# Performance work log

Measured on AMD Instinct MI355X. Metric: run time of the kernel, lower is better.

## Reference

```python
import jax, jax.numpy as jnp
import numpy as np
from jax import lax

# SSD300/COCO geometry
B, P, C = 16, 8732, 81
V_CENTER, V_SIZE = 0.1, 0.2        # box coder variances
SCORE_THRESH = 0.05
NMS_THRESH = 0.45
DETS_PER_IMG = 100
PRE_NMS_TOPK = 1000                # fixed-size candidate set for jit-compatible NMS
MIN_SIZE = 0.01                    # remove_small_boxes threshold


def setup_inputs() -> dict:
    key = jax.random.key(0)
    k1, k2, k3, k4, k5 = jax.random.split(key, 5)
    # scale logits so a realistic fraction of softmax scores clears SCORE_THRESH
    pred_logits = jax.random.normal(k1, (B, P, C), jnp.float32) * 2.0
    pred_boxes = jax.random.normal(k2, (B, P, 4), jnp.float32) * 0.5
    # priors in (cx, cy, w, h), normalized coords, positive sizes
    cxcy = jax.random.uniform(k3, (P, 2), jnp.float32, 0.05, 0.95)
    wh = jax.random.uniform(k4, (P, 2), jnp.float32, 0.02, 0.4)
    priors = jnp.concatenate([cxcy, wh], axis=-1)
    target_sizes = jax.random.randint(k5, (B, 2), 480, 1333)  # (h, w) per image
    return {"pred_logits": pred_logits, "pred_boxes": pred_boxes,
            "priors": priors, "target_sizes": target_sizes}


def _decode(rel, priors):
    # SSD box coder: rel = (dx, dy, dw, dh), priors = (cx, cy, w, h) -> xyxy
    cxcy = priors[:, :2] + rel[:, :2] * V_CENTER * priors[:, 2:]
    wh = priors[:, 2:] * jnp.exp(rel[:, 2:] * V_SIZE)
    return jnp.concatenate([cxcy - 0.5 * wh, cxcy + 0.5 * wh], axis=-1)


def _pairwise_iou(b):
    # b: [K, 4] xyxy
    area = (b[:, 2] - b[:, 0]) * (b[:, 3] - b[:, 1])
    lt = jnp.maximum(b[:, None, :2], b[None, :, :2])
    rb = jnp.minimum(b[:, None, 2:], b[None, :, 2:])
    whi = jnp.clip(rb - lt, 0.0)
    inter = whi[..., 0] * whi[..., 1]
    return inter / (area[:, None] + area[None, :] - inter + 1e-9)


def _per_image(logits, rel, priors, size_hw):
    nc1 = C - 1  # foreground classes
    # decode and scale to pixel coords: target_size.flip(0).repeat(2) = [w, h, w, h]
    size_hw = size_hw.astype(jnp.float32)
    whwh = jnp.concatenate([size_hw[::-1], size_hw[::-1]])
    boxes = _decode(rel, priors) * whwh                     # [P, 4]
    scores = jax.nn.softmax(logits, axis=-1)[:, 1:]          # [P, C-1], drop background
    # score threshold + remove_small_boxes, fused as a mask (jit-safe)
    size_ok = ((boxes[:, 2] - boxes[:, 0]) >= MIN_SIZE) & \
              ((boxes[:, 3] - boxes[:, 1]) >= MIN_SIZE)      # [P]
    valid = (scores > SCORE_THRESH) & size_ok[:, None]       # [P, C-1]
    s_flat = jnp.where(valid, scores, -1.0).reshape(-1)      # [P*(C-1)]
    vals, idx = lax.top_k(s_flat, PRE_NMS_TOPK)
    prior_idx = idx // nc1
    labels_k = idx % nc1 + 1                                 # class ids in [1, C)
    boxes_k = boxes[prior_idx]                               # [K, 4]
    vmask = vals > 0.0                                       # real candidates
    # batched_nms via per-class coordinate offset
    max_coord = jnp.max(jnp.where(vmask[:, None], boxes_k, 0.0))
    offs_boxes = boxes_k + (labels_k.astype(jnp.float32) * (max_coord + 1.0))[:, None]
    iou = _pairwise_iou(offs_boxes)                          # [K, K]
    cols = jnp.arange(PRE_NMS_TOPK)

    def body(i, keep):
        suppress = (iou[i] > NMS_THRESH) & keep[i] & (cols > i)
        return keep & ~suppress

    keep = lax.fori_loop(0, PRE_NMS_TOPK, body, vmask)
    kept_scores = jnp.where(keep, vals, -1.0)
    fvals, fidx = lax.top_k(kept_scores, DETS_PER_IMG)
    fvalid = fvals > 0.0
    out_boxes = jnp.where(fvalid[:, None], boxes_k[fidx], 0.0)
    out_scores = jnp.where(fvalid, fvals, 0.0)
    out_labels = jnp.where(fvalid, labels_k[fidx], -1)
    return out_boxes, out_scores, out_labels


def reference(pred_logits, pred_boxes, priors, target_sizes):
    boxes, scores, labels = jax.vmap(_per_image, in_axes=(0, 0, None, 0))(
        pred_logits, pred_boxes, priors, target_sizes)
    # padded, fixed-size equivalent of the per-image list of dicts
    return boxes, scores, labels
```

## Files before the change

### kernel.cpp

```cpp
#include <hip/hip_runtime.h>
#include <math.h>

#pragma clang fp contract(off)

#define NIMG 16
#define NP   8732
#define NCLS 81
#define NFG  80
#define KTOP 1000
#define KPAD 1024
#define DETS 100
#define CAPMAX 166912
#define BASEBITS 0x3D000000u
#define CNT_STRIDE 64
#define TILEB 137
#define NB 640

#define OFF_BOXES  0u
#define OFF_CNT    2235392u
#define OFF_GHIST  2239488u
#define OFF_CSCORE 2280448u
#define OFF_CLABEL 2345984u
#define OFF_CBOX   2411520u
#define OFF_COFFS  2673664u
#define OFF_CAREA  2935808u
#define OFF_VALIDW 3001344u
#define OFF_MASK   3003392u
#define OFF_CAND   5100544u
#define MEMSET_LEN 45056u

typedef unsigned long long u64;
typedef unsigned int u32;

#define AS_GLOBAL __attribute__((address_space(1)))
#define AS_LOCAL  __attribute__((address_space(3)))

__global__ __launch_bounds__(256, 6) void k_decode(
    const float* __restrict__ logits, const float* __restrict__ rel,
    const float* __restrict__ priors, const int* __restrict__ tsz,
    float* __restrict__ boxes_out, u64* __restrict__ cand,
    u32* __restrict__ cnt, u32* __restrict__ ghist, int cap)
{
#pragma clang fp contract(off)
    __shared__ __align__(16) float lx[64 * NCLS];
    __shared__ float pmx[4 * 64];
    __shared__ float psm[4 * 64];
    __shared__ u32 sok[64];
    __shared__ u32 wtt[4];
    __shared__ u32 sbase;
    __shared__ u32 lhist[NB];
    int b  = blockIdx.x / TILEB;
    int g  = blockIdx.x - b * TILEB;
    int p0 = g * 64;
    int t  = threadIdx.x;
    int lane = t & 63;
    int q = t >> 6;
    int npri = NP - p0; if (npri > 64) npri = 64;
    int words = npri * NCLS;

    const u32* s32 = (const u32*)(logits + ((size_t)b * NP + p0) * NCLS);
    u32* lxw = (u32*)lx;
    int full = words >> 8;
    for (int k = q; k < full; k += 4)
        __builtin_amdgcn_global_load_lds(
            (AS_GLOBAL const u32*)(s32 + (k << 8) + (lane << 2)),
            (AS_LOCAL u32*)(lxw + (k << 8)), 16, 0, 0);
    int base = full << 8;
    int c4 = (words - base) >> 6;
    for (int k = q; k < c4; k += 4)
        __builtin_amdgcn_global_load_lds(
            (AS_GLOBAL const u32*)(s32 + base + (k << 6) + lane),
            (AS_LOCAL u32*)(lxw + base + (k << 6)), 4, 0, 0);
    int base2 = base + (c4 << 6);
    if (q == 0 && lane < words - base2) lxw[base2 + lane] = s32[base2 + lane];

    for (int i = t; i < NB; i += 256) lhist[i] = 0;

    int p = p0 + lane;
    bool active = p < NP;

    if (q == 0) {
        u32 ok = 0;
        if (active) {
            float4 pr = ((const float4*)priors)[p];
            float4 rl = ((const float4*)rel)[(size_t)b * NP + p];
            float W = (float)tsz[b * 2 + 1], H = (float)tsz[b * 2 + 0];
            float cx = pr.x + (rl.x * 0.1f) * pr.z;
            float cy = pr.y + (rl.y * 0.1f) * pr.w;
            float w_ = pr.z * expf(rl.z * 0.2f);
            float h_ = pr.w * expf(rl.w * 0.2f);
            float4 bx;
            bx.x = (cx - 0.5f * w_) * W; bx.y = (cy - 0.5f * h_) * H;
            bx.z = (cx + 0.5f * w_) * W; bx.w = (cy + 0.5f * h_) * H;
            ((float4*)boxes_out)[(size_t)b * NP + p] = bx;
            ok = ((bx.z - bx.x) >= 0.01f) && ((bx.w - bx.y) >= 0.01f);
        }
        sok[lane] = ok;
    }
    __syncthreads();

    int tb = lane * NCLS;
    int nk = (q == 0) ? 21 : 20;
    float x[21];
    #pragma unroll
    for (int k = 0; k < 21; ++k) {
        int c = q + 4 * k;
        x[k] = (k < nk) ? lx[tb + c] : -3.4e38f;
    }
    float pm = -3.4e38f;
    #pragma unroll
    for (int k = 0; k < 21; ++k) if (k < nk) pm = fmaxf(pm, x[k]);
    pmx[q * 64 + lane] = pm;
    __syncthreads();
    float m = fmaxf(fmaxf(pmx[lane], pmx[64 + lane]),
                    fmaxf(pmx[128 + lane], pmx[192 + lane]));

    float ps = 0.f;
    #pragma unroll
    for (int k = 0; k < 21; ++k) {
        if (k < nk) { x[k] = expf(x[k] - m); ps += x[k]; }
    }
    psm[q * 64 + lane] = ps;
    __syncthreads();
    float s = (psm[lane] + psm[64 + lane]) + (psm[128 + lane] + psm[192 + lane]);

    float hi = 0.05000075f * s;
    float lo = 0.04999925f * s;
    u32 pass = 0, band = 0;
    u32 sizeok = sok[lane];
    if (active && sizeok) {
        #pragma unroll
        for (int k = 0; k < 21; ++k) {
            int c = q + 4 * k;
            if (k < nk && c >= 1) {
                bool pa = x[k] > hi;
                bool bd = (!pa) && (x[k] > lo);
                pass |= ((u32)pa) << k;
                band |= ((u32)bd) << k;
            }
        }
    }
    while (band) {
        int k = __builtin_ctz(band); band &= band - 1;
        int c = q + 4 * k;
        float e = expf(lx[tb + c] - m);
        if (e / s > 0.05f) pass |= 1u << k;
    }
    int cnt_t = __popc(pass);

    int pre = cnt_t;
    #pragma unroll
    for (int d = 1; d < 64; d <<= 1) {
        int o = __shfl_up(pre, d);
        if (lane >= d) pre += o;
    }
    if (lane == 63) wtt[q] = (u32)pre;
    __syncthreads();
    u32 before = 0;
    for (int w = 0; w < 4; ++w) if (w < q) before += wtt[w];
    if (t == 0) {
        u32 tot = wtt[0] + wtt[1] + wtt[2] + wtt[3];
        sbase = tot ? atomicAdd(cnt + b * CNT_STRIDE, tot) : 0u;
    }
    __syncthreads();
    u32 pos = sbase + before + (u32)(pre - cnt_t);

    u64* cb = cand + (size_t)b * cap;
    u32 flatneg = 0xFFFFFFFFu - (u32)p * NFG;
    while (pass) {
        int k = __builtin_ctz(pass); pass &= pass - 1;
        int c = q + 4 * k;
        float e = expf(lx[tb + c] - m);
        float d = e / s;
        if ((int)pos < cap) {
            u32 sb = __float_as_uint(d);
            cb[pos] = ((u64)sb << 32) | (u64)(flatneg - (u32)(c - 1));
            u32 bin = (sb - BASEBITS) >> 16; if (bin > NB - 1) bin = NB - 1;
            atomicAdd(&lhist[bin], 1u);
        }
        ++pos;
    }
    __syncthreads();
    u32* gh = ghist + b * NB;
    for (int i = t; i < NB; i += 256) {
        u32 v = lhist[i];
        if (v) atomicAdd(gh + i, v);
    }
}

__device__ __forceinline__ void suffix_find(
    u32* hist, u32* wt, u32 K, int tid,
    volatile int* outI, volatile u32* outNext)
{
    int lane = tid & 63, w = tid >> 6;
    u32 v[8]; u32 tot = 0;
    #pragma unroll
    for (int k = 0; k < 8; ++k) { v[k] = hist[tid * 8 + k]; tot += v[k]; }
    u32 ws = tot;
    #pragma unroll
    for (int d = 1; d < 64; d <<= 1) {
        u32 o = __shfl_down(ws, d);
        if (lane + d < 64) ws += o;
    }
    if (lane == 0) wt[w] = ws;
    __syncthreads();
    u32 tail = 0;
    for (int w2 = w + 1; w2 < 16; ++w2) tail += wt[w2];
    u32 after = (ws - tot) + tail;
    u32 sufk[9];
    sufk[8] = after;
    #pragma unroll
    for (int k = 7; k >= 0; --k) sufk[k] = v[k] + sufk[k + 1];
    #pragma unroll
    for (int k = 0; k < 8; ++k) {
        if (sufk[k] >= K && sufk[k + 1] < K) {
            *outI = tid * 8 + k;
            *outNext = sufk[k + 1];
        }
    }
    __syncthreads();
}

__global__ __launch_bounds__(1024) void k_select(
    const u64* __restrict__ cand, const u32* __restrict__ cnt,
    const u32* __restrict__ ghist, const float* __restrict__ boxes,
    float* __restrict__ cscore, int* __restrict__ clabel,
    float4* __restrict__ cbox, float4* __restrict__ coffs,
    float* __restrict__ carea, u64* __restrict__ validw, int cap)
{
#pragma clang fp contract(off)
    __shared__ u32 h[NB];
    __shared__ u32 fh[8192];
    __shared__ u32 wt[16];
    __shared__ u64 buf[2048];
    __shared__ float red16[16];
    __shared__ int sh_c, sh_i2;
    __shared__ u32 sh_S, sh_next, sh_d, sh_m;
    int b = blockIdx.x, t = threadIdx.x, lane = t & 63;
    u32 n = min(cnt[b * CNT_STRIDE], (u32)cap);
    const u64* cb = cand + (size_t)b * cap;

    for (int i = t; i < NB; i += 1024) h[i] = ghist[b * NB + i];
    if (t == 0) { sh_c = -2; sh_i2 = -2; sh_S = 0; sh_next = 0; sh_m = 0; }
    __syncthreads();
    if (t < 64) {
        u32 v[10]; u32 tot = 0;
        #pragma unroll
        for (int k = 0; k < 10; ++k) { v[k] = h[t * 10 + k]; tot += v[k]; }
        u32 ws = tot;
        #pragma unroll
        for (int d = 1; d < 64; d <<= 1) {
            u32 o = (u32)__shfl_down((int)ws, d);
            if (t + d < 64) ws += o;
        }
        u32 suf[11];
        suf[10] = ws - tot;
        #pragma unroll
        for (int k = 9; k >= 0; --k) suf[k] = v[k] + suf[k + 1];
        #pragma unroll
        for (int k = 0; k < 10; ++k) {
            if (suf[k] >= (u32)KTOP && suf[k + 1] < (u32)KTOP) {
                sh_c = t * 10 + k; sh_S = suf[k]; sh_next = suf[k + 1];
            }
        }
    }
    __syncthreads();
    int c = sh_c;
    u32 T = 0;
    if (c >= 0) {
        u32 Tc = BASEBITS + ((u32)c << 16);
        if (sh_S <= 2048u) {
            T = Tc;
        } else {
            u32 nhi = sh_next;
            for (int i = t; i < 8192; i += 1024) fh[i] = 0;
            __syncthreads();
            for (u32 i = (u32)t; i < n; i += 1024) {
                u32 sb = (u32)(cb[i] >> 32);
                if ((sb & 0xFFFF0000u) == Tc)
                    atomicAdd(&fh[(sb >> 3) & 0x1FFFu], 1u);
            }
            __syncthreads();
            suffix_find(fh, wt, (u32)KTOP - nhi, t, &sh_i2, &sh_d);
            T = (sh_i2 >= 0) ? (Tc + ((u32)sh_i2 << 3)) : Tc;
        }
    }
    for (u32 bs0 = 0; bs0 < n; bs0 += 8192) {
        u64 kk[8];
        bool qq[8];
        #pragma unroll
        for (int e = 0; e < 8; ++e) {
            u32 idx = bs0 + (u32)t + ((u32)e << 10);
            qq[e] = idx < n;
            kk[e] = 0ULL;
            if (qq[e]) kk[e] = cb[idx];
        }
        #pragma unroll
        for (int e = 0; e < 8; ++e) {
            bool pick = qq[e] && ((u32)(kk[e] >> 32) >= T);
            u64 bal = __ballot(pick);
            u32 wb = 0;
            if (lane == 0 && bal) wb = atomicAdd(&sh_m, (u32)__popcll(bal));
            wb = (u32)__shfl((int)wb, 0);
            if (pick) {
                u32 pos = wb + (u32)__popcll(bal & ((1ULL << lane) - 1ULL));
                if (pos < 2048) buf[pos] = kk[e];
            }
        }
    }
    __syncthreads();
    u32 m = min(sh_m, 2048u);
    for (int i = t; i < 2048; i += 1024) if ((u32)i >= m) buf[i] = 0ULL;
    __syncthreads();
    for (int k = 2; k <= 2048; k <<= 1) {
        for (int j = k >> 1; j >= 64; j >>= 1) {
            #pragma unroll
            for (int e = 0; e < 2; ++e) {
                int i = t + e * 1024;
                int ixj = i ^ j;
                if (ixj > i) {
                    u64 a = buf[i], bb = buf[ixj];
                    bool up = (i & k) == 0;
                    if (up ? (a < bb) : (a > bb)) { buf[i] = bb; buf[ixj] = a; }
                }
            }
            __syncthreads();
        }
        u64 v0 = buf[t], v1 = buf[t + 1024];
        bool up0 = (t & k) == 0;
        bool up1 = ((t + 1024) & k) == 0;
        int js = ((k >> 1) < 32) ? (k >> 1) : 32;
        for (int j = js; j >= 1; j >>= 1) {
            u64 o0 = __shfl_xor(v0, j);
            u64 o1 = __shfl_xor(v1, j);
            bool lo0 = (t & j) == 0;
            v0 = (lo0 == up0) ? (v0 > o0 ? v0 : o0) : (v0 < o0 ? v0 : o0);
            v1 = (lo0 == up1) ? (v1 > o1 ? v1 : o1) : (v1 < o1 ? v1 : o1);
        }
        buf[t] = v0; buf[t + 1024] = v1;
        __syncthreads();
    }
    u64 key = (t < KTOP) ? buf[t] : 0ULL;
    float s = __uint_as_float((u32)(key >> 32));
    bool valid = s > 0.0f;
    u32 flat = valid ? (0xFFFFFFFFu - (u32)key) : 0u;
    int prior = (int)(flat / NFG);
    int cls = (int)(flat - (u32)prior * NFG) + 1;
    float4 bx = make_float4(0.f, 0.f, 0.f, 0.f);
    if (valid) bx = ((const float4*)boxes)[b * NP + prior];
    cscore[b * KPAD + t] = s;
    clabel[b * KPAD + t] = cls;
    cbox[b * KPAD + t] = bx;
    u64 vb = __ballot(valid);
    if (lane == 0) validw[b * 16 + (t >> 6)] = vb;
    float lm = valid ? fmaxf(fmaxf(bx.x, bx.y), fmaxf(bx.z, bx.w)) : 0.0f;
    lm = fmaxf(lm, 0.0f);
    #pragma unroll
    for (int d = 1; d < 64; d <<= 1) lm = fmaxf(lm, __shfl_xor(lm, d));
    if (lane == 0) red16[t >> 6] = lm;
    __syncthreads();
    float mc = red16[0];
    #pragma unroll
    for (int w = 1; w < 16; ++w) mc = fmaxf(mc, red16[w]);
    float off = (float)cls * (mc + 1.0f);
    float4 ob = valid ? make_float4(bx.x + off, bx.y + off, bx.z + off, bx.w + off)
                      : make_float4(0.f, 0.f, 0.f, 0.f);
    float area = valid ? (ob.z - ob.x) * (ob.w - ob.y) : 0.0f;
    coffs[b * KPAD + t] = ob;
    carea[b * KPAD + t] = area;
}

__global__ __launch_bounds__(1024) void k_iou(
    const float4* __restrict__ coffs, const float* __restrict__ carea,
    u64* __restrict__ cmask)
{
#pragma clang fp contract(off)
    __shared__ float4 bs[KPAD];
    __shared__ float as_[KPAD];
    int b = blockIdx.x >> 4, tile = blockIdx.x & 15;
    int t = threadIdx.x;
    bs[t] = coffs[b * KPAD + t];
    as_[t] = carea[b * KPAD + t];
    __syncthreads();
    int j = tile * 64 + (t & 63);
    int w = t >> 6;
    float4 bj = bs[j];
    float aj = as_[j];
    int r0 = w * 64;
    u64 bits = 0;
    #pragma unroll 4
    for (int k = 0; k < 64; ++k) {
        int r = r0 + k;
        float4 br = bs[r];
        float ar = as_[r];
        float ltx = fmaxf(br.x, bj.x), lty = fmaxf(br.y, bj.y);
        float rbx = fminf(br.z, bj.z), rby = fminf(br.w, bj.w);
        float wx = fmaxf(rbx - ltx, 0.0f), wy = fmaxf(rby - lty, 0.0f);
        float inter = wx * wy;
        float denom = ((ar + aj) - inter) + 1e-9f;
        float iou = inter / denom;
        bool sup = (iou > 0.45f) && (j > r);
        bits |= ((u64)sup) << k;
    }
    cmask[((size_t)b * 16 + w) * KPAD + j] = bits;
}

__global__ __launch_bounds__(1024) void k_nms(
    const u64* __restrict__ cmask, const u64* __restrict__ validw,
    const float* __restrict__ cscore, const int* __restrict__ clabel,
    const float4* __restrict__ cbox, float* __restrict__ out)
{
    __shared__ __align__(16) u64 smask[16 * KPAD];
    __shared__ u64 sk[16];
    __shared__ int pfx[17];
    __shared__ int slot[DETS];
    int b = blockIdx.x, t = threadIdx.x, lane = t & 63;

    {
        const float4* cm4 = (const float4*)(cmask + (size_t)b * 16 * KPAD);
        float4* sm4 = (float4*)smask;
        #pragma unroll
        for (int i = 0; i < 8; ++i) sm4[t + (i << 10)] = cm4[t + (i << 10)];
    }
    __syncthreads();

    if (t < 64) {
        u64 kept[16];
        #pragma unroll
        for (int g = 0; g < 16; ++g) {
            u64 vg = validw[b * 16 + g];
            bool rem = false;
            #pragma unroll
            for (int w2 = 0; w2 < 16; ++w2)
                if (w2 < g)
                    rem |= (kept[w2] & smask[w2 * KPAD + g * 64 + lane]) != 0ULL;
            u64 cg = smask[g * KPAD + g * 64 + lane];
            bool myv = ((vg >> lane) & 1ULL) && !rem;
            u64 K = __ballot(myv);
            for (;;) {
                u64 K2 = __ballot(myv && ((K & cg) == 0ULL));
                if (K2 == K) break;
                K = K2;
            }
            kept[g] = K;
        }
        if (lane == 0) {
            int run = 0;
            #pragma unroll
            for (int l = 0; l < 16; ++l) {
                sk[l] = kept[l]; pfx[l] = run; run += __popcll(kept[l]);
            }
            pfx[16] = run;
        }
    }
    __syncthreads();
    if (t < 16) {
        int r = pfx[t];
        u64 wv = sk[t];
        while (wv && r < DETS) {
            int bit = __builtin_ctzll(wv);
            slot[r] = t * 64 + bit;
            ++r;
            wv &= wv - 1;
        }
    }
    __syncthreads();
    int total = min(pfx[16], DETS);
    if (t < DETS) {
        int r = t;
        float4 bx = make_float4(0.f, 0.f, 0.f, 0.f);
        float s = 0.0f;
        int lb = -1;
        if (r < total) {
            int cdx = slot[r];
            bx = cbox[b * KPAD + cdx];
            s = cscore[b * KPAD + cdx];
            lb = clabel[b * KPAD + cdx];
        }
        float* ob = out + ((size_t)b * DETS + r) * 4;
        ob[0] = bx.x; ob[1] = bx.y; ob[2] = bx.z; ob[3] = bx.w;
        out[NIMG * DETS * 4 + b * DETS + r] = s;
        out[NIMG * DETS * 4 + NIMG * DETS + b * DETS + r] = (float)lb;
    }
}

extern "C" void kernel_launch(void* const* d_in, const int* in_sizes, int n_in,
                              void* d_out, int out_size, void* d_ws, size_t ws_size,
                              hipStream_t stream) {
    const float* logits = (const float*)d_in[0];
    const float* rel    = (const float*)d_in[1];
    const float* priors = (const float*)d_in[2];
    const int*   tsz    = (const int*)d_in[3];
    float* out = (float*)d_out;
    char* ws = (char*)d_ws;

    float* boxes  = (float*)(ws + OFF_BOXES);
    u32*   cnt    = (u32*)(ws + OFF_CNT);
    u32*   ghist  = (u32*)(ws + OFF_GHIST);
    float* cscore = (float*)(ws + OFF_CSCORE);
    int*   clabel = (int*)(ws + OFF_CLABEL);
    float4* cbox  = (float4*)(ws + OFF_CBOX);
    float4* coffs = (float4*)(ws + OFF_COFFS);
    float* carea  = (float*)(ws + OFF_CAREA);
    u64*   validw = (u64*)(ws + OFF_VALIDW);
    u64*   cmask  = (u64*)(ws + OFF_MASK);
    u64*   cand   = (u64*)(ws + OFF_CAND);

    long long avail = ((long long)ws_size - (long long)OFF_CAND) / (NIMG * 8);
    int cap = (int)(avail < CAPMAX ? (avail > 0 ? avail : 1) : CAPMAX);
    cap &= ~1;

    hipMemsetAsync(cnt, 0, MEMSET_LEN, stream);
    k_decode<<<NIMG * TILEB, 256, 0, stream>>>(logits, rel, priors, tsz,
                                               boxes, cand, cnt, ghist, cap);
    k_select<<<NIMG, 1024, 0, stream>>>(cand, cnt, ghist, boxes, cscore, clabel,
                                        cbox, coffs, carea, validw, cap);
    k_iou<<<NIMG * 16, 1024, 0, stream>>>(coffs, carea, cmask);
    k_nms<<<NIMG, 1024, 0, stream>>>(cmask, validw, cscore, clabel, cbox, out);
}
```

Baseline: 154.0 us.

## Prefetch candidates in select, use per-wave atomics, interleave images across blocks

Measured after the change: 154.8 us. No clear change (+0.5%).

```diff
diff --git a/kernel.cpp b/kernel.cpp
--- a/kernel.cpp
+++ b/kernel.cpp
@@ -46,11 +46,9 @@
     __shared__ float pmx[4 * 64];
     __shared__ float psm[4 * 64];
     __shared__ u32 sok[64];
-    __shared__ u32 wtt[4];
-    __shared__ u32 sbase;
     __shared__ u32 lhist[NB];
-    int b  = blockIdx.x / TILEB;
-    int g  = blockIdx.x - b * TILEB;
+    int b  = blockIdx.x & 15;
+    int g  = blockIdx.x >> 4;
     int p0 = g * 64;
     int t  = threadIdx.x;
     int lane = t & 63;
@@ -154,16 +152,11 @@
         int o = __shfl_up(pre, d);
         if (lane >= d) pre += o;
     }
-    if (lane == 63) wtt[q] = (u32)pre;
-    __syncthreads();
-    u32 before = 0;
-    for (int w = 0; w < 4; ++w) if (w < q) before += wtt[w];
-    if (t == 0) {
-        u32 tot = wtt[0] + wtt[1] + wtt[2] + wtt[3];
-        sbase = tot ? atomicAdd(cnt + b * CNT_STRIDE, tot) : 0u;
-    }
-    __syncthreads();
-    u32 pos = sbase + before + (u32)(pre - cnt_t);
+    u32 wbase = 0;
+    if (lane == 63 && pre > 0)
+        wbase = atomicAdd(cnt + b * CNT_STRIDE, (u32)pre);
+    wbase = (u32)__shfl((int)wbase, 63);
+    u32 pos = wbase + (u32)(pre - cnt_t);
 
     u64* cb = cand + (size_t)b * cap;
     u32 flatneg = 0xFFFFFFFFu - (u32)p * NFG;
@@ -239,6 +232,16 @@
     int b = blockIdx.x, t = threadIdx.x, lane = t & 63;
     u32 n = min(cnt[b * CNT_STRIDE], (u32)cap);
     const u64* cb = cand + (size_t)b * cap;
+    const float4* cb4 = (const float4*)cb;
+
+    float4 cur[4]; bool unused_cq;
+    #pragma unroll
+    for (int e = 0; e < 4; ++e) {
+        u32 p2 = (u32)(e << 10) + (u32)t;
+        cur[e] = make_float4(0.f, 0.f, 0.f, 0.f);
+        if ((p2 << 1) < n) cur[e] = cb4[p2];
+    }
+    (void)unused_cq;
 
     for (int i = t; i < NB; i += 1024) h[i] = ghist[b * NB + i];
     if (t == 0) { sh_c = -2; sh_i2 = -2; sh_S = 0; sh_next = 0; sh_m = 0; }
@@ -286,27 +289,45 @@
         }
     }
     for (u32 bs0 = 0; bs0 < n; bs0 += 8192) {
-        u64 kk[8];
-        bool qq[8];
-        #pragma unroll
-        for (int e = 0; e < 8; ++e) {
-            u32 idx = bs0 + (u32)t + ((u32)e << 10);
-            qq[e] = idx < n;
-            kk[e] = 0ULL;
-            if (qq[e]) kk[e] = cb[idx];
-        }
-        #pragma unroll
-        for (int e = 0; e < 8; ++e) {
-            bool pick = qq[e] && ((u32)(kk[e] >> 32) >= T);
-            u64 bal = __ballot(pick);
+        u32 bs1 = bs0 + 8192;
+        float4 nxt[4];
+        if (bs1 < n) {
+            #pragma unroll
+            for (int e = 0; e < 4; ++e) {
+                u32 p2 = (bs1 >> 1) + (u32)(e << 10) + (u32)t;
+                nxt[e] = make_float4(0.f, 0.f, 0.f, 0.f);
+                if ((p2 << 1) < n) nxt[e] = cb4[p2];
+            }
+        } else {
+            #pragma unroll
+            for (int e = 0; e < 4; ++e) nxt[e] = make_float4(0.f, 0.f, 0.f, 0.f);
+        }
+        #pragma unroll
+        for (int e = 0; e < 4; ++e) {
+            u32 gk = bs0 + (((u32)(e << 10) + (u32)t) << 1);
+            u64 k0 = ((u64)__float_as_uint(cur[e].y) << 32) | (u64)__float_as_uint(cur[e].x);
+            u64 k1 = ((u64)__float_as_uint(cur[e].w) << 32) | (u64)__float_as_uint(cur[e].z);
+            bool pick0 = (gk < n)     && ((u32)(k0 >> 32) >= T);
+            bool pick1 = (gk + 1 < n) && ((u32)(k1 >> 32) >= T);
+            u64 bal0 = __ballot(pick0);
             u32 wb = 0;
-            if (lane == 0 && bal) wb = atomicAdd(&sh_m, (u32)__popcll(bal));
+            if (lane == 0 && bal0) wb = atomicAdd(&sh_m, (u32)__popcll(bal0));
             wb = (u32)__shfl((int)wb, 0);
-            if (pick) {
-                u32 pos = wb + (u32)__popcll(bal & ((1ULL << lane) - 1ULL));
-                if (pos < 2048) buf[pos] = kk[e];
-            }
-        }
+            if (pick0) {
+                u32 pos = wb + (u32)__popcll(bal0 & ((1ULL << lane) - 1ULL));
+                if (pos < 2048) buf[pos] = k0;
+            }
+            u64 bal1 = __ballot(pick1);
+            u32 wb1 = 0;
+            if (lane == 0 && bal1) wb1 = atomicAdd(&sh_m, (u32)__popcll(bal1));
+            wb1 = (u32)__shfl((int)wb1, 0);
+            if (pick1) {
+                u32 pos = wb1 + (u32)__popcll(bal1 & ((1ULL << lane) - 1ULL));
+                if (pos < 2048) buf[pos] = k1;
+            }
+        }
+        #pragma unroll
+        for (int e = 0; e < 4; ++e) cur[e] = nxt[e];
     }
     __syncthreads();
     u32 m = min(sh_m, 2048u);
@@ -377,7 +398,7 @@
 #pragma clang fp contract(off)
     __shared__ float4 bs[KPAD];
     __shared__ float as_[KPAD];
-    int b = blockIdx.x >> 4, tile = blockIdx.x & 15;
+    int b = blockIdx.x & 15, tile = blockIdx.x >> 4;
     int t = threadIdx.x;
     bs[t] = coffs[b * KPAD + t];
     as_[t] = carea[b * KPAD + t];
```
